# Kernel optimization log

Measured on AMD Instinct MI355X. Metric: run time of the kernel, lower is better.

The kernel has to match this reference:

```python
import jax, jax.numpy as jnp
import numpy as np

M_PER_GROUP = 16
ITER_NUM = 5
EPS = 1e-3


def _iter_norm_whiten(sigma, iter_num=ITER_NUM):
    """Newton-Schulz iteration for Sigma^{-1/2}. sigma: (G, m, m)."""
    g, m, _ = sigma.shape
    eye = jnp.eye(m, dtype=sigma.dtype)
    # normalize by trace so spectral radius < 1
    trace = jnp.trace(sigma, axis1=1, axis2=2)[:, None, None]  # (G,1,1)
    sigma_n = sigma / trace
    P = jnp.broadcast_to(eye, (g, m, m))
    for _ in range(iter_num):
        P3 = P @ P @ P
        P = 1.5 * P - 0.5 * (P3 @ sigma_n)
    # whitening matrix: Sigma^{-1/2} = P / sqrt(trace)
    return P * jax.lax.rsqrt(trace)


def setup_inputs() -> dict:
    key = jax.random.key(0)
    inputs = jax.random.normal(key, (64, 56, 56, 256), dtype=jnp.float32)
    return {"inputs": inputs}


def reference(inputs) -> jnp.ndarray:
    b, w, h, c = inputs.shape
    group = c // M_PER_GROUP
    # center: channels-first flatten, subtract per-channel batch mean
    x = jnp.transpose(inputs, (3, 0, 1, 2)).reshape(c, -1)  # (c, N)
    m = jnp.mean(x, axis=1, keepdims=True)                  # (c, 1)
    f = x - m
    n = f.shape[1]
    fg = f.reshape(group, M_PER_GROUP, n)                   # (G, m, N)
    # per-group covariance
    cov = jnp.einsum('gmn,gkn->gmk', fg, fg) / n            # (G, m, m)
    eye = jnp.eye(M_PER_GROUP, dtype=inputs.dtype)
    sigma = (1.0 - EPS) * cov + EPS * eye
    wm = _iter_norm_whiten(sigma)                           # (G, m, m)
    # whiten
    f_hat = wm @ fg                                         # (G, m, N)
    decorrelated = f_hat.reshape(c, b, w, h)
    return jnp.transpose(decorrelated, (1, 2, 3, 0))        # (b, w, h, c)
```

## Files before the change

### kernel.cpp

```cpp
#include <hip/hip_runtime.h>


constexpr int CCH = 256;
constexpr float EPSV = 1e-3f;
constexpr int PSTRIDE = 4352;
constexpr int STATBLK = 1024;

typedef float f32x4 __attribute__((ext_vector_type(4)));
typedef unsigned int u32;

__device__ __forceinline__ void gload16(const float* g, float* l) {
    __builtin_amdgcn_global_load_lds(
        (const __attribute__((address_space(1))) u32*)g,
        (__attribute__((address_space(3))) u32*)l, 16, 0, 0);
}

#define WAIT4 asm volatile("s_waitcnt vmcnt(4)" ::: "memory")
#define WAIT0 asm volatile("s_waitcnt vmcnt(0)" ::: "memory")

#define QB(S, comp) __int_as_float(__builtin_amdgcn_update_dpp( \
    0, __float_as_int(comp), (S) * 0x55, 0xF, 0xF, 1))
#define ROT1(comp) __int_as_float(__builtin_amdgcn_update_dpp( \
    0, __float_as_int(comp), 0x39, 0xF, 0xF, 1))
#define ROT2(comp) __int_as_float(__builtin_amdgcn_update_dpp( \
    0, __float_as_int(comp), 0x4E, 0xF, 0xF, 1))

#define FMA4(C, V, U) \
    { C.x += (V).x * (U); C.y += (V).y * (U); C.z += (V).z * (U); C.w += (V).w * (U); }

#define ACCPOS(V)                                                         \
    {                                                                     \
        ss.x += (V).x; ss.y += (V).y; ss.z += (V).z; ss.w += (V).w;       \
        d0 += (V).x * (V).x; d1 += (V).x * (V).y;                         \
        d2 += (V).x * (V).z; d3 += (V).x * (V).w;                         \
        d4 += (V).y * (V).y; d5 += (V).y * (V).z;                         \
        d6 += (V).y * (V).w; d7 += (V).z * (V).z;                         \
        d8 += (V).z * (V).w; d9 += (V).w * (V).w;                         \
        {                                                                 \
            float4 u;                                                     \
            u.x = ROT1((V).x); u.y = ROT1((V).y);                         \
            u.z = ROT1((V).z); u.w = ROT1((V).w);                         \
            FMA4(mA, u, (V).x) FMA4(mB, u, (V).y)                         \
            FMA4(mC, u, (V).z) FMA4(mD, u, (V).w)                         \
        }                                                                 \
        {                                                                 \
            float4 u;                                                     \
            u.x = ROT2((V).x); u.y = ROT2((V).y);                         \
            u.z = ROT2((V).z); u.w = ROT2((V).w);                         \
            FMA4(nA, u, (V).x) FMA4(nB, u, (V).y)                         \
            FMA4(nC, u, (V).z) FMA4(nD, u, (V).w)                         \
        }                                                                 \
    }

#define SW(RI, CJ, VAL)  sl[gbase + (RI) * 16 + (CJ)] = (VAL);
#define SWM(RI, CJ, VAL) { sl[gbase + (RI) * 16 + (CJ)] = (VAL); \
                           sl[gbase + (CJ) * 16 + (RI)] = (VAL); }
#define SR(RI, CJ, VAR)  VAR += sl[gbase + (RI) * 16 + (CJ)];

#define SLOT_WRITE()                                                        \
    {                                                                       \
        const int R = 4 * rr, A = 4 * c1, B = 4 * c2;                       \
        SW(R+0, R+0, d0) SWM(R+0, R+1, d1) SWM(R+0, R+2, d2)                \
        SWM(R+0, R+3, d3) SW(R+1, R+1, d4) SWM(R+1, R+2, d5)                \
        SWM(R+1, R+3, d6) SW(R+2, R+2, d7) SWM(R+2, R+3, d8)                \
        SW(R+3, R+3, d9)                                                    \
        SWM(R+0, A+0, mA.x) SWM(R+0, A+1, mA.y) SWM(R+0, A+2, mA.z)         \
        SWM(R+0, A+3, mA.w) SWM(R+1, A+0, mB.x) SWM(R+1, A+1, mB.y)         \
        SWM(R+1, A+2, mB.z) SWM(R+1, A+3, mB.w) SWM(R+2, A+0, mC.x)         \
        SWM(R+2, A+1, mC.y) SWM(R+2, A+2, mC.z) SWM(R+2, A+3, mC.w)         \
        SWM(R+3, A+0, mD.x) SWM(R+3, A+1, mD.y) SWM(R+3, A+2, mD.z)         \
        SWM(R+3, A+3, mD.w)                                                 \
        SW(R+0, B+0, nA.x) SW(R+0, B+1, nA.y) SW(R+0, B+2, nA.z)            \
        SW(R+0, B+3, nA.w) SW(R+1, B+0, nB.x) SW(R+1, B+1, nB.y)            \
        SW(R+1, B+2, nB.z) SW(R+1, B+3, nB.w) SW(R+2, B+0, nC.x)            \
        SW(R+2, B+1, nC.y) SW(R+2, B+2, nC.z) SW(R+2, B+3, nC.w)            \
        SW(R+3, B+0, nD.x) SW(R+3, B+1, nD.y) SW(R+3, B+2, nD.z)            \
        SW(R+3, B+3, nD.w)                                                  \
        sl[4160 + lane * 4 + 0] = ss.x; sl[4160 + lane * 4 + 1] = ss.y;     \
        sl[4160 + lane * 4 + 2] = ss.z; sl[4160 + lane * 4 + 3] = ss.w;     \
    }

#define SLOT_ADD()                                                          \
    {                                                                       \
        const int R = 4 * rr, A = 4 * c1, B = 4 * c2;                       \
        SR(R+0, R+0, d0) SR(R+0, R+1, d1) SR(R+0, R+2, d2)                  \
        SR(R+0, R+3, d3) SR(R+1, R+1, d4) SR(R+1, R+2, d5)                  \
        SR(R+1, R+3, d6) SR(R+2, R+2, d7) SR(R+2, R+3, d8)                  \
        SR(R+3, R+3, d9)                                                    \
        SR(R+0, A+0, mA.x) SR(R+0, A+1, mA.y) SR(R+0, A+2, mA.z)            \
        SR(R+0, A+3, mA.w) SR(R+1, A+0, mB.x) SR(R+1, A+1, mB.y)            \
        SR(R+1, A+2, mB.z) SR(R+1, A+3, mB.w) SR(R+2, A+0, mC.x)            \
        SR(R+2, A+1, mC.y) SR(R+2, A+2, mC.z) SR(R+2, A+3, mC.w)            \
        SR(R+3, A+0, mD.x) SR(R+3, A+1, mD.y) SR(R+3, A+2, mD.z)            \
        SR(R+3, A+3, mD.w)                                                  \
        SR(R+0, B+0, nA.x) SR(R+0, B+1, nA.y) SR(R+0, B+2, nA.z)            \
        SR(R+0, B+3, nA.w) SR(R+1, B+0, nB.x) SR(R+1, B+1, nB.y)            \
        SR(R+1, B+2, nB.z) SR(R+1, B+3, nB.w) SR(R+2, B+0, nC.x)            \
        SR(R+2, B+1, nC.y) SR(R+2, B+2, nC.z) SR(R+2, B+3, nC.w)            \
        SR(R+3, B+0, nD.x) SR(R+3, B+1, nD.y) SR(R+3, B+2, nD.z)            \
        SR(R+3, B+3, nD.w)                                                  \
        ss.x += sl[4160 + lane * 4 + 0]; ss.y += sl[4160 + lane * 4 + 1];   \
        ss.z += sl[4160 + lane * 4 + 2]; ss.w += sl[4160 + lane * 4 + 3];   \
    }

#define ISSUE(BUF, C)                                                       \
    {                                                                       \
        const float* gp = x + (size_t)(start + 4 * (C)) * CCH + lane * 4;   \
        gload16(gp,           (BUF));                                       \
        gload16(gp + CCH,     (BUF) + 256);                                 \
        gload16(gp + 2 * CCH, (BUF) + 512);                                 \
        gload16(gp + 3 * CCH, (BUF) + 768);                                 \
    }

#define PROC(BUF)                                                           \
    {                                                                       \
        const float4 v0 = *reinterpret_cast<const float4*>((BUF) + lane * 4);        \
        const float4 v1 = *reinterpret_cast<const float4*>((BUF) + 256 + lane * 4);  \
        const float4 v2 = *reinterpret_cast<const float4*>((BUF) + 512 + lane * 4);  \
        const float4 v3 = *reinterpret_cast<const float4*>((BUF) + 768 + lane * 4);  \
        ACCPOS(v0); ACCPOS(v1); ACCPOS(v2); ACCPOS(v3);                     \
    }

__global__ __launch_bounds__(256, 4) void k_stats(const float* __restrict__ x,
                                                  float* __restrict__ partial,
                                                  int npos) {
    const int tid = threadIdx.x;
    const int lane = tid & 63;
    const int w = tid >> 6;
    const int wid = blockIdx.x * 4 + w;
    const int nwaves = gridDim.x * 4;
    const int g = lane >> 2;
    const int rr = lane & 3;
    const int c1 = (rr + 1) & 3;
    const int c2 = (rr + 2) & 3;
    const int gbase = g * 260;

    float4 ss = {0.f, 0.f, 0.f, 0.f};
    float d0 = 0.f, d1 = 0.f, d2 = 0.f, d3 = 0.f, d4 = 0.f, d5 = 0.f,
          d6 = 0.f, d7 = 0.f, d8 = 0.f, d9 = 0.f;
    float4 mA = ss, mB = ss, mC = ss, mD = ss;
    float4 nA = ss, nB = ss, nC = ss, nD = ss;

    __shared__ float lds[8192];
    float* b0 = &lds[w * 2048];
    float* b1 = b0 + 1024;

    const int cpw = (npos + nwaves - 1) / nwaves;
    const int start = wid * cpw;
    const int end = (start + cpw < npos) ? start + cpw : npos;
    const int n = (end > start) ? end - start : 0;
    const int nf4 = n >> 2;

    if (nf4 >= 2) {
        ISSUE(b0, 0);
        ISSUE(b1, 1);
        int i = 0;
        for (; i + 2 < nf4; ++i) {
            WAIT4;
            float* bb = (i & 1) ? b1 : b0;
            PROC(bb);
            ISSUE(bb, i + 2);
        }
        WAIT4;
        PROC(((i & 1) ? b1 : b0));
        ++i;
        WAIT0;
        PROC(((i & 1) ? b1 : b0));
    } else if (nf4 == 1) {
        ISSUE(b0, 0);
        WAIT0;
        PROC(b0);
    }
    for (int q = start + 4 * nf4; q < end; ++q) {
        const float4 v = *reinterpret_cast<const float4*>(x + (size_t)q * CCH + lane * 4);
        ACCPOS(v);
    }

    float* sl = lds;
    __syncthreads();

    if (w == 1) SLOT_WRITE();
    __syncthreads();
    if (w == 0) SLOT_ADD();
    __syncthreads();
    if (w == 3) SLOT_WRITE();
    __syncthreads();
    if (w == 2) SLOT_ADD();
    __syncthreads();
    if (w == 2) SLOT_WRITE();
    __syncthreads();
    if (w == 0) { SLOT_ADD(); SLOT_WRITE(); }
    __syncthreads();

    float* rec = partial + (size_t)blockIdx.x * PSTRIDE;
    for (int c = tid; c < 256; c += blockDim.x)
        rec[c] = sl[4160 + c];
    for (int e = tid; e < 4096; e += blockDim.x) {
        const int gg = e >> 8, row = (e >> 4) & 15, col = e & 15;
        rec[256 + e] = sl[gg * 260 + row * 16 + col];
    }
}

__global__ __launch_bounds__(256) void k_reduce1(const float* __restrict__ partial,
                                                 float* __restrict__ p2,
                                                 int nblk, int nchunks) {
    const int t = blockIdx.x * blockDim.x + threadIdx.x;
    const int total = nchunks * PSTRIDE;
    if (t >= total) return;
    const int chunk = t / PSTRIDE;
    const int e = t - chunk * PSTRIDE;
    const int r0 = chunk * 64;
    const int rend = (r0 + 64 < nblk) ? r0 + 64 : nblk;
    const float* src = partial + (size_t)r0 * PSTRIDE + e;
    float acc = 0.f;
    for (int r = r0; r < rend; ++r, src += PSTRIDE) acc += *src;
    p2[(size_t)chunk * PSTRIDE + e] = acc;
}

__global__ __launch_bounds__(256) void k_wm(const float* __restrict__ p2,
                                            int nchunks,
                                            float* __restrict__ mean,
                                            float* __restrict__ wm,
                                            float inv_n) {
    const int g = blockIdx.x;
    const int tid = threadIdx.x;
    const int i = tid >> 4;
    const int j = tid & 15;

    __shared__ float mu[16];
    __shared__ float sig[16][17];
    __shared__ float P[16][17];
    __shared__ float T[16][17];
    __shared__ float U[16][17];

    float cs = 0.f;
    {
        const float* s = p2 + 256 + g * 256 + i * 16 + j;
        for (int c = 0; c < nchunks; ++c, s += PSTRIDE) cs += *s;
    }
    if (tid < 16) {
        float ms = 0.f;
        const float* s = p2 + g * 16 + tid;
        for (int c = 0; c < nchunks; ++c, s += PSTRIDE) ms += *s;
        const float m = ms * inv_n;
        mu[tid] = m;
        mean[g * 16 + tid] = m;
    }
    __syncthreads();

    const float cov = cs * inv_n - mu[i] * mu[j];
    const float s = (1.0f - EPSV) * cov + ((i == j) ? EPSV : 0.0f);
    sig[i][j] = s;
    __syncthreads();

    float tr = 0.f;
#pragma unroll
    for (int k = 0; k < 16; ++k) tr += sig[k][k];
    __syncthreads();

    sig[i][j] = s / tr;
    P[i][j] = (i == j) ? 1.0f : 0.0f;
    __syncthreads();

    for (int it = 0; it < 5; ++it) {
        float a = 0.f;
#pragma unroll
        for (int k = 0; k < 16; ++k) a += P[i][k] * P[k][j];
        T[i][j] = a;
        __syncthreads();

        float b = 0.f;
#pragma unroll
        for (int k = 0; k < 16; ++k) b += T[i][k] * P[k][j];
        U[i][j] = b;
        __syncthreads();

        float c = 0.f;
#pragma unroll
        for (int k = 0; k < 16; ++k) c += U[i][k] * sig[k][j];
        const float pn = 1.5f * P[i][j] - 0.5f * c;
        __syncthreads();
        P[i][j] = pn;
        __syncthreads();
    }

    wm[(g * 16 + i) * 16 + j] = P[i][j] * rsqrtf(tr);
}

__global__ __launch_bounds__(256) void k_whiten(const float* __restrict__ x,
                                                const float* __restrict__ mean,
                                                const float* __restrict__ wm,
                                                float* __restrict__ out,
                                                int npos) {
    const int tid = threadIdx.x;
    const int lane = tid & 63;
    const int wave = blockIdx.x * (blockDim.x >> 6) + (tid >> 6);
    const int nwaves = gridDim.x * (blockDim.x >> 6);
    const int g = lane >> 2;
    const int i0 = (lane & 3) * 4;

    float w[4][16];
    const float* wg = wm + g * 256;
#pragma unroll
    for (int a = 0; a < 4; ++a)
#pragma unroll
        for (int j = 0; j < 16; ++j) w[a][j] = wg[(i0 + a) * 16 + j];

    const float4 mu4 = *reinterpret_cast<const float4*>(mean + lane * 4);
    const float* bx = x + lane * 4;
    float* bo = out + lane * 4;

    int p = wave;
    if (p >= npos) return;
    float4 v = *reinterpret_cast<const float4*>(bx + (size_t)p * CCH);
    while (true) {
        const int pn = p + nwaves;
        const bool more = pn < npos;
        float4 vn = v;
        if (more) vn = *reinterpret_cast<const float4*>(bx + (size_t)pn * CCH);

        v.x -= mu4.x; v.y -= mu4.y; v.z -= mu4.z; v.w -= mu4.w;
        float acc[4] = {0.f, 0.f, 0.f, 0.f};
#define WSTEP(S)                                                         \
        {                                                                \
            const float u0 = QB(S, v.x), u1 = QB(S, v.y),                \
                        u2 = QB(S, v.z), u3 = QB(S, v.w);                \
            _Pragma("unroll")                                            \
            for (int a = 0; a < 4; ++a) {                                \
                acc[a] += w[a][(S) * 4 + 0] * u0 + w[a][(S) * 4 + 1] * u1 \
                        + w[a][(S) * 4 + 2] * u2 + w[a][(S) * 4 + 3] * u3; \
            }                                                            \
        }
        WSTEP(0) WSTEP(1) WSTEP(2) WSTEP(3)
#undef WSTEP
        f32x4 o;
        o.x = acc[0]; o.y = acc[1]; o.z = acc[2]; o.w = acc[3];
        __builtin_nontemporal_store(o, reinterpret_cast<f32x4*>(bo + (size_t)p * CCH));

        if (!more) break;
        p = pn;
        v = vn;
    }
}

extern "C" void kernel_launch(void* const* d_in, const int* in_sizes, int n_in,
                              void* d_out, int out_size, void* d_ws, size_t ws_size,
                              hipStream_t stream) {
    const float* x = (const float*)d_in[0];
    float* out = (float*)d_out;
    float* ws = (float*)d_ws;

    const int total = in_sizes[0];
    const int npos = total / CCH;
    const float inv_n = 1.0f / (float)npos;

    float* mean = ws + 4352;
    float* wm = ws + 4608;
    float* partial = ws + 8704;

    long avail = (long)(ws_size / 4) - 8704 - 16 * PSTRIDE;
    int nblk = (int)(avail / PSTRIDE);
    if (nblk > STATBLK) nblk = STATBLK;
    if (nblk < 64) nblk = 64;

    float* p2 = partial + (size_t)nblk * PSTRIDE;

    k_stats<<<nblk, 256, 0, stream>>>(x, partial, npos);
    const int nchunks = (nblk + 63) / 64;
    const int r1threads = nchunks * PSTRIDE;
    k_reduce1<<<(r1threads + 255) / 256, 256, 0, stream>>>(partial, p2, nblk, nchunks);
    k_wm<<<16, 256, 0, stream>>>(p2, nchunks, mean, wm, inv_n);
    k_whiten<<<2048, 256, 0, stream>>>(x, mean, wm, out, npos);
}
```

Measured before the change: 138.3 us.

## Pipeline whiten pass with async global-to-LDS double buffering over contiguous chunks

The whitening kernel now gives each wave a contiguous range of positions and streams them through a per-wave double-buffered LDS staging area, loaded with global_load_lds and synchronised with vmcnt waits. This keeps several loads in flight in place of the previous one-ahead register prefetch with a strided loop, and the grid is halved. It relies on the ISSUE macro defined earlier in the file and adds 32KB of LDS per block, which can limit occupancy.

```diff
diff --git a/kernel.cpp b/kernel.cpp
--- a/kernel.cpp
+++ b/kernel.cpp
@@ -15,6 +15,7 @@
         (__attribute__((address_space(3))) u32*)l, 16, 0, 0);
 }
 
+#define WAIT8 asm volatile("s_waitcnt vmcnt(8)" ::: "memory")
 #define WAIT4 asm volatile("s_waitcnt vmcnt(4)" ::: "memory")
 #define WAIT0 asm volatile("s_waitcnt vmcnt(0)" ::: "memory")
 
@@ -287,59 +288,109 @@
     wm[(g * 16 + i) * 16 + j] = P[i][j] * rsqrtf(tr);
 }
 
-__global__ __launch_bounds__(256) void k_whiten(const float* __restrict__ x,
-                                                const float* __restrict__ mean,
-                                                const float* __restrict__ wm,
-                                                float* __restrict__ out,
-                                                int npos) {
+#define WQ(S)                                                               \
+    {                                                                       \
+        const float u0 = QB(S, vv.x), u1 = QB(S, vv.y),                     \
+                    u2 = QB(S, vv.z), u3 = QB(S, vv.w);                     \
+        a0 += wr[0][(S) * 4 + 0] * u0 + wr[0][(S) * 4 + 1] * u1             \
+            + wr[0][(S) * 4 + 2] * u2 + wr[0][(S) * 4 + 3] * u3;            \
+        a1 += wr[1][(S) * 4 + 0] * u0 + wr[1][(S) * 4 + 1] * u1             \
+            + wr[1][(S) * 4 + 2] * u2 + wr[1][(S) * 4 + 3] * u3;            \
+        a2 += wr[2][(S) * 4 + 0] * u0 + wr[2][(S) * 4 + 1] * u1             \
+            + wr[2][(S) * 4 + 2] * u2 + wr[2][(S) * 4 + 3] * u3;            \
+        a3 += wr[3][(S) * 4 + 0] * u0 + wr[3][(S) * 4 + 1] * u1             \
+            + wr[3][(S) * 4 + 2] * u2 + wr[3][(S) * 4 + 3] * u3;            \
+    }
+
+#define WPOS(V, POSIDX)                                                     \
+    {                                                                       \
+        float4 vv = (V);                                                    \
+        vv.x -= mu4.x; vv.y -= mu4.y; vv.z -= mu4.z; vv.w -= mu4.w;         \
+        float a0 = 0.f, a1 = 0.f, a2 = 0.f, a3 = 0.f;                       \
+        WQ(0) WQ(1) WQ(2) WQ(3)                                             \
+        f32x4 o;                                                            \
+        o.x = a0; o.y = a1; o.z = a2; o.w = a3;                             \
+        __builtin_nontemporal_store(o,                                      \
+            reinterpret_cast<f32x4*>(out + (size_t)(POSIDX) * CCH + lane * 4)); \
+    }
+
+#define WPROC(BUF, C)                                                       \
+    {                                                                       \
+        const int pbase = start + 4 * (C);                                  \
+        const float4 v0 = *reinterpret_cast<const float4*>((BUF) + lane * 4);        \
+        const float4 v1 = *reinterpret_cast<const float4*>((BUF) + 256 + lane * 4);  \
+        const float4 v2 = *reinterpret_cast<const float4*>((BUF) + 512 + lane * 4);  \
+        const float4 v3 = *reinterpret_cast<const float4*>((BUF) + 768 + lane * 4);  \
+        WPOS(v0, pbase) WPOS(v1, pbase + 1)                                 \
+        WPOS(v2, pbase + 2) WPOS(v3, pbase + 3)                             \
+    }
+
+__global__ __launch_bounds__(256, 4) void k_whiten(const float* __restrict__ x,
+                                                   const float* __restrict__ mean,
+                                                   const float* __restrict__ wm,
+                                                   float* __restrict__ out,
+                                                   int npos) {
     const int tid = threadIdx.x;
     const int lane = tid & 63;
-    const int wave = blockIdx.x * (blockDim.x >> 6) + (tid >> 6);
-    const int nwaves = gridDim.x * (blockDim.x >> 6);
+    const int w = tid >> 6;
+    const int wid = blockIdx.x * 4 + w;
+    const int nwaves = gridDim.x * 4;
     const int g = lane >> 2;
     const int i0 = (lane & 3) * 4;
 
-    float w[4][16];
+    float wr[4][16];
     const float* wg = wm + g * 256;
 #pragma unroll
     for (int a = 0; a < 4; ++a)
 #pragma unroll
-        for (int j = 0; j < 16; ++j) w[a][j] = wg[(i0 + a) * 16 + j];
+        for (int j = 0; j < 16; ++j) wr[a][j] = wg[(i0 + a) * 16 + j];
 
     const float4 mu4 = *reinterpret_cast<const float4*>(mean + lane * 4);
-    const float* bx = x + lane * 4;
-    float* bo = out + lane * 4;
-
-    int p = wave;
-    if (p >= npos) return;
-    float4 v = *reinterpret_cast<const float4*>(bx + (size_t)p * CCH);
-    while (true) {
-        const int pn = p + nwaves;
-        const bool more = pn < npos;
-        float4 vn = v;
-        if (more) vn = *reinterpret_cast<const float4*>(bx + (size_t)pn * CCH);
-
-        v.x -= mu4.x; v.y -= mu4.y; v.z -= mu4.z; v.w -= mu4.w;
-        float acc[4] = {0.f, 0.f, 0.f, 0.f};
-#define WSTEP(S)                                                         \
-        {                                                                \
-            const float u0 = QB(S, v.x), u1 = QB(S, v.y),                \
-                        u2 = QB(S, v.z), u3 = QB(S, v.w);                \
-            _Pragma("unroll")                                            \
-            for (int a = 0; a < 4; ++a) {                                \
-                acc[a] += w[a][(S) * 4 + 0] * u0 + w[a][(S) * 4 + 1] * u1 \
-                        + w[a][(S) * 4 + 2] * u2 + w[a][(S) * 4 + 3] * u3; \
-            }                                                            \
+
+    __shared__ float lds[8192];
+    float* b0 = &lds[w * 2048];
+    float* b1 = b0 + 1024;
+
+    const int cpw = (npos + nwaves - 1) / nwaves;
+    const int start = wid * cpw;
+    const int end = (start + cpw < npos) ? start + cpw : npos;
+    const int n = (end > start) ? end - start : 0;
+    const int nf4 = n >> 2;
+
+    if (nf4 >= 2) {
+        ISSUE(b0, 0);
+        ISSUE(b1, 1);
+        int i = 0;
+        if (i + 2 < nf4) {
+            WAIT4;
+            WPROC(b0, 0);
+            ISSUE(b0, 2);
+            ++i;
+            for (; i + 2 < nf4; ++i) {
+                WAIT8;
+                float* bb = (i & 1) ? b1 : b0;
+                WPROC(bb, i);
+                ISSUE(bb, i + 2);
+            }
+            WAIT8;
+            WPROC(((i & 1) ? b1 : b0), i);
+            ++i;
+            WAIT4;
+            WPROC(((i & 1) ? b1 : b0), i);
+        } else {
+            WAIT4;
+            WPROC(b0, 0);
+            WAIT4;
+            WPROC(b1, 1);
         }
-        WSTEP(0) WSTEP(1) WSTEP(2) WSTEP(3)
-#undef WSTEP
-        f32x4 o;
-        o.x = acc[0]; o.y = acc[1]; o.z = acc[2]; o.w = acc[3];
-        __builtin_nontemporal_store(o, reinterpret_cast<f32x4*>(bo + (size_t)p * CCH));
-
-        if (!more) break;
-        p = pn;
-        v = vn;
+    } else if (nf4 == 1) {
+        ISSUE(b0, 0);
+        WAIT0;
+        WPROC(b0, 0);
+    }
+    for (int q = start + 4 * nf4; q < end; ++q) {
+        const float4 v = *reinterpret_cast<const float4*>(x + (size_t)q * CCH + lane * 4);
+        WPOS(v, q);
     }
 }
 
@@ -370,5 +421,5 @@
     const int r1threads = nchunks * PSTRIDE;
     k_reduce1<<<(r1threads + 255) / 256, 256, 0, stream>>>(partial, p2, nblk, nchunks);
     k_wm<<<16, 256, 0, stream>>>(p2, nchunks, mean, wm, inv_n);
-    k_whiten<<<2048, 256, 0, stream>>>(x, mean, wm, out, npos);
-}
+    k_whiten<<<1024, 256, 0, stream>>>(x, mean, wm, out, npos);
+}
```

Result: slower. 182.8 us (+32.2%).
